# Optimization experiments

Measured on AMD Instinct MI355X. Metric: run time of the kernel, lower is better.

Reference implementation:

```python
import jax, jax.numpy as jnp
import numpy as np

LARGE_NUMBER = 10000.0   # Always rnn-cell init value
NEG_FILL = -1000000.0    # RHS fill for j < i (from torch.ones(...) * -1000000)


def _minish(x, scale, axis):
    # torch Minish: softmin-weighted sum if scale > 0 else hard min
    if scale > 0:
        return jnp.sum(jax.nn.softmax(-x * scale, axis=axis) * x, axis=axis)
    return jnp.min(x, axis=axis)


def _maxish(x, scale, axis):
    # torch Maxish: softmax-weighted sum if scale > 0 else hard max
    if scale > 0:
        return jnp.sum(jax.nn.softmax(x * scale, axis=axis) * x, axis=axis)
    return jnp.max(x, axis=axis)


def _until(trace1, trace2, scale):
    # trace1, trace2: [B, T, X]
    B, T, X = trace1.shape
    idx = jnp.arange(T)

    # RHS[b, j, x, i] = Always(trace1[:, i:, :]) at relative step j - i
    #                 = min(LARGE_NUMBER, min_{k=i..j} trace1[b, k, x])   for j >= i
    # Computed in ONE pass with lax.scan over time j, carrying the running
    # min for every start index i (reset at i == j). Entries i > j are
    # garbage and masked to NEG_FILL afterwards (matching torch's -1e6 fill).
    def step(r, inp):
        j, t1j = inp                      # t1j: [B, X]
        t1b = t1j[:, None, :]             # [B, 1, X]
        is_start = (idx[None, :, None] == j)
        r = jnp.where(is_start,
                      jnp.minimum(LARGE_NUMBER, t1b),   # reset: min(h0, x_j)
                      jnp.minimum(r, t1b))              # running min
        return r, r

    r0 = jnp.full((B, T, X), LARGE_NUMBER, dtype=trace1.dtype)
    _, Ms = jax.lax.scan(step, r0, (idx, jnp.transpose(trace1, (1, 0, 2))))
    # Ms: [j, B, i, X] -> RHS: [B, j, x, i]
    RHS = jnp.transpose(Ms, (1, 0, 3, 2))
    valid = idx[None, :, None, None] >= idx[None, None, None, :]  # j >= i
    RHS = jnp.where(valid, RHS, NEG_FILL)

    # LHS[b, j, x, i] = trace2[b, i, x]  (broadcast over j)
    LHS = jnp.broadcast_to(jnp.transpose(trace2, (0, 2, 1))[:, None, :, :], RHS.shape)

    # min over {LHS, RHS} pair, then max over candidate start times i
    inner = _minish(jnp.stack([LHS, RHS], axis=-1), scale, -1)  # [B, j, x, i]
    return _maxish(inner, scale, -1)                            # [B, T, X]


def setup_inputs() -> dict:
    key = jax.random.key(0)
    k1, k2 = jax.random.split(key)
    B, T, X = 16, 512, 8
    trace1 = jax.random.normal(k1, (B, T, X), dtype=jnp.float32)
    trace2 = jax.random.normal(k2, (B, T, X), dtype=jnp.float32)
    return {"trace1": trace1, "trace2": trace2, "scale": 0}


def reference(trace1, trace2, scale):
    return _until(trace1, trace2, scale)
```

## Files before the change

kernel.cpp:

```cpp
#include <hip/hip_runtime.h>
#include <math.h>


#define B_DIM 16
#define T_DIM 512
#define X_DIM 8

__global__ __launch_bounds__(64) void until_scan_kernel(
    const float* __restrict__ t1, const float* __restrict__ t2,
    float* __restrict__ out)
{
    const int wave = blockIdx.x;
    const int lane = threadIdx.x;
    const int b = wave >> 3;
    const int x = wave & 7;

    const size_t base = (size_t)b * T_DIM * X_DIM + x;
    const int t0 = lane * 8;

    float av[8], cv[8];
#pragma unroll
    for (int k = 0; k < 8; ++k) {
        av[k] = t1[base + (size_t)(t0 + k) * X_DIM];
        cv[k] = t2[base + (size_t)(t0 + k) * X_DIM];
    }

    float C = -INFINITY, A = INFINITY;
#pragma unroll
    for (int k = 0; k < 8; ++k) {
        A = fminf(fmaxf(A, cv[k]), av[k]);
        C = fmaxf(C, cv[k]);
    }

#pragma unroll
    for (int d = 1; d < 64; d <<= 1) {
        float Cp = __shfl_up(C, d, 64);
        float Ap = __shfl_up(A, d, 64);
        if (lane >= d) {
            A = fminf(fmaxf(Ap, C), A);
            C = fmaxf(Cp, C);
        }
    }

    float Cex = __shfl_up(C, 1, 64);
    float Aex = __shfl_up(A, 1, 64);
    if (lane == 0) { Cex = -INFINITY; Aex = INFINITY; }

    float f = fminf(Cex, Aex);
#pragma unroll
    for (int k = 0; k < 8; ++k) {
        f = fminf(fmaxf(f, cv[k]), av[k]);
        out[base + (size_t)(t0 + k) * X_DIM] = f;
    }
}

extern "C" void kernel_launch(void* const* d_in, const int* in_sizes, int n_in,
                              void* d_out, int out_size, void* d_ws, size_t ws_size,
                              hipStream_t stream) {
    const float* trace1 = (const float*)d_in[0];
    const float* trace2 = (const float*)d_in[1];
    float* out = (float*)d_out;

    until_scan_kernel<<<B_DIM * X_DIM, 64, 0, stream>>>(trace1, trace2, out);
}
```

Baseline: 57.46 us.

## Stage batch tile through LDS for coalesced float4 loads and stores

Each block now handles a whole batch (all 8 channels, 512 threads) instead of one wave per (batch, channel). Inputs are loaded with coalesced float4 reads, transposed through padded shared memory, scanned per channel by one wave each, then written back through shared memory as coalesced float4 stores. This targets the strided global accesses of the old layout. The trade-off is fewer blocks (16 instead of 128), two barriers and extra LDS traffic.

```diff
diff --git a/kernel.cpp b/kernel.cpp
--- a/kernel.cpp
+++ b/kernel.cpp
@@ -6,23 +6,55 @@
 #define T_DIM 512
 #define X_DIM 8
 
-__global__ __launch_bounds__(64) void until_scan_kernel(
+#define GSTRIDE 9
+#define KSTRIDE (64 * GSTRIDE)
+#define LDS_WORDS (8 * KSTRIDE)
+
+__device__ __forceinline__ int lds_idx(int t, int x) {
+    return (t & 7) * KSTRIDE + (t >> 3) * GSTRIDE + x;
+}
+
+__global__ __launch_bounds__(512) void until_scan_kernel(
     const float* __restrict__ t1, const float* __restrict__ t2,
     float* __restrict__ out)
 {
-    const int wave = blockIdx.x;
-    const int lane = threadIdx.x;
-    const int b = wave >> 3;
-    const int x = wave & 7;
+    __shared__ float sa[LDS_WORDS];
+    __shared__ float sc[LDS_WORDS];
+    __shared__ float sf[LDS_WORDS];
 
-    const size_t base = (size_t)b * T_DIM * X_DIM + x;
-    const int t0 = lane * 8;
+    const int b   = blockIdx.x;
+    const int tid = threadIdx.x;
+    const size_t base = (size_t)b * (T_DIM * X_DIM);
+
+    const float4* a4 = (const float4*)(t1 + base);
+    const float4* c4 = (const float4*)(t2 + base);
+
+    float4 va0 = a4[tid];
+    float4 vc0 = c4[tid];
+    float4 va1 = a4[tid + 512];
+    float4 vc1 = c4[tid + 512];
+
+#pragma unroll
+    for (int i = 0; i < 2; ++i) {
+        const int idx = tid + i * 512;
+        const float4 va = (i == 0) ? va0 : va1;
+        const float4 vc = (i == 0) ? vc0 : vc1;
+        const int t = idx >> 1;
+        const int x = (idx & 1) * 4;
+        const int o = lds_idx(t, x);
+        sa[o]     = va.x; sa[o + 1] = va.y; sa[o + 2] = va.z; sa[o + 3] = va.w;
+        sc[o]     = vc.x; sc[o + 1] = vc.y; sc[o + 2] = vc.z; sc[o + 3] = vc.w;
+    }
+    __syncthreads();
+
+    const int lane = tid & 63;
+    const int x    = tid >> 6;
 
     float av[8], cv[8];
 #pragma unroll
     for (int k = 0; k < 8; ++k) {
-        av[k] = t1[base + (size_t)(t0 + k) * X_DIM];
-        cv[k] = t2[base + (size_t)(t0 + k) * X_DIM];
+        av[k] = sa[k * KSTRIDE + lane * GSTRIDE + x];
+        cv[k] = sc[k * KSTRIDE + lane * GSTRIDE + x];
     }
 
     float C = -INFINITY, A = INFINITY;
@@ -50,7 +82,20 @@
 #pragma unroll
     for (int k = 0; k < 8; ++k) {
         f = fminf(fmaxf(f, cv[k]), av[k]);
-        out[base + (size_t)(t0 + k) * X_DIM] = f;
+        sf[k * KSTRIDE + lane * GSTRIDE + x] = f;
+    }
+    __syncthreads();
+
+    float4* o4 = (float4*)(out + base);
+#pragma unroll
+    for (int i = 0; i < 2; ++i) {
+        const int idx = tid + i * 512;
+        const int t = idx >> 1;
+        const int x0 = (idx & 1) * 4;
+        const int o = lds_idx(t, x0);
+        float4 v;
+        v.x = sf[o]; v.y = sf[o + 1]; v.z = sf[o + 2]; v.w = sf[o + 3];
+        o4[idx] = v;
     }
 }
 
@@ -61,5 +106,5 @@
     const float* trace2 = (const float*)d_in[1];
     float* out = (float*)d_out;
 
-    until_scan_kernel<<<B_DIM * X_DIM, 64, 0, stream>>>(trace1, trace2, out);
+    until_scan_kernel<<<B_DIM, 512, 0, stream>>>(trace1, trace2, out);
 }
```

Result: no change. 58.52 us (+1.8%).
